# Performance work log

Hardware: AMD Instinct MI355X
Metric: run time of the kernel (lower is better)

## Reference

```python
import jax, jax.numpy as jnp
import numpy as np

LN_EPS = 1e-5

def _ln(x, g, b):
    mu = x.mean(-1, keepdims=True)
    var = ((x - mu) ** 2).mean(-1, keepdims=True)
    return (x - mu) * jax.lax.rsqrt(var + LN_EPS) * g + b

def _gru(x, h, wih, whh, bih, bhh):
    # torch GRUCell: gates ordered (r, z, n)
    gi = x @ wih.T + bih
    gh = h @ whh.T + bhh
    ir, iz, inn = jnp.split(gi, 3, axis=-1)
    hr, hz, hn = jnp.split(gh, 3, axis=-1)
    r = jax.nn.sigmoid(ir + hr)
    z = jax.nn.sigmoid(iz + hz)
    n = jnp.tanh(inn + r * hn)
    return (1.0 - z) * n + z * h

def setup_inputs() -> dict:
    key = jax.random.key(0)
    ks = jax.random.split(key, 10)
    B, N, D, S, H = 64, 4096, 128, 8, 256
    w = D ** -0.5  # weight scale to keep activations sane
    return {
        'inputs': jax.random.normal(ks[0], (B, N, D), jnp.float32),
        'slot_noise': jax.random.normal(ks[1], (1, S, D), jnp.float32),
        'slots_mu': jax.random.normal(ks[2], (1, S, D), jnp.float32) * w,
        'slots_log_sigma': jnp.zeros((1, S, D), jnp.float32),
        'wq': jax.random.normal(ks[3], (D, D), jnp.float32) * w,
        'bq': jnp.zeros((D,), jnp.float32),
        'wk': jax.random.normal(ks[4], (D, D), jnp.float32) * w,
        'bk': jnp.zeros((D,), jnp.float32),
        'wv': jax.random.normal(ks[5], (D, D), jnp.float32) * w,
        'bv': jnp.zeros((D,), jnp.float32),
        'gru_wih': jax.random.normal(ks[6], (3 * D, D), jnp.float32) * w,
        'gru_whh': jax.random.normal(ks[7], (3 * D, D), jnp.float32) * w,
        'gru_bih': jnp.zeros((3 * D,), jnp.float32),
        'gru_bhh': jnp.zeros((3 * D,), jnp.float32),
        'ns_g': jnp.ones((D,), jnp.float32),
        'ns_b': jnp.zeros((D,), jnp.float32),
        'ni_g': jnp.ones((D,), jnp.float32),
        'ni_b': jnp.zeros((D,), jnp.float32),
        'mlp_ln_g': jnp.ones((D,), jnp.float32),
        'mlp_ln_b': jnp.zeros((D,), jnp.float32),
        'mlp_w1': jax.random.normal(ks[8], (H, D), jnp.float32) * w,
        'mlp_b1': jnp.zeros((H,), jnp.float32),
        'mlp_w2': jax.random.normal(ks[9], (D, H), jnp.float32) * (H ** -0.5),
        'mlp_b2': jnp.zeros((D,), jnp.float32),
    }

N_ITERS = 3

def reference(inputs, slot_noise, slots_mu, slots_log_sigma, wq, bq, wk, bk, wv, bv,
              gru_wih, gru_whh, gru_bih, gru_bhh, ns_g, ns_b, ni_g, ni_b,
              mlp_ln_g, mlp_ln_b, mlp_w1, mlp_b1, mlp_w2, mlp_b2):
    B, N, D = inputs.shape
    S = slots_mu.shape[1]
    slots = slots_mu + jnp.exp(slots_log_sigma) * slot_noise  # [1,S,D]
    slots = jnp.broadcast_to(slots, (B, S, D))
    x = _ln(inputs, ni_g, ni_b)
    k = x @ wk.T + bk  # [B,N,D]
    v = x @ wv.T + bv
    scale = 1.0 / jnp.sqrt(jnp.float32(D))
    for _ in range(N_ITERS):
        q = _ln(slots, ns_g, ns_b) @ wq.T + bq  # [B,S,D]
        logits = jnp.einsum('bnd,bsd->bns', k, q) * scale
        attn = jax.nn.softmax(logits, axis=-1)  # softmax over slots
        attn_norm = jnp.clip(attn.sum(axis=1, keepdims=True), 1e-8, None)
        slot_attn = attn / attn_norm
        updates = jnp.einsum('bns,bnd->bsd', slot_attn, v)
        slots = _gru(updates, slots, gru_wih, gru_whh, gru_bih, gru_bhh)
        h = jax.nn.gelu(_ln(slots, mlp_ln_g, mlp_ln_b) @ mlp_w1.T + mlp_b1, approximate=False)
        slots = slots + (h @ mlp_w2.T + mlp_b2)
    return slots
```

## Files before the change

### kernel.cpp

```cpp
#include <hip/hip_runtime.h>
#include <hip/hip_bf16.h>
#include <math.h>

#define Bn 64
#define Nn 4096
#define Dn 128
#define Sn 8
#define Hn 256
#define LN_EPS 1e-5f
#define QSCALE 0.08838834764831845f

typedef __bf16 bf16x8 __attribute__((ext_vector_type(8)));
typedef float f32x4 __attribute__((ext_vector_type(4)));
typedef unsigned short ushort_t;

__device__ __forceinline__ float dot4(float4 a, float4 b) {
    return a.x*b.x + a.y*b.y + a.z*b.z + a.w*b.w;
}
__device__ __forceinline__ ushort_t f2bf(float f) {
    __bf16 b = (__bf16)f;
    ushort_t u; __builtin_memcpy(&u, &b, 2); return u;
}
__device__ __forceinline__ float bf2f(ushort_t u) {
    unsigned int x = ((unsigned int)u) << 16; float f; __builtin_memcpy(&f, &x, 4); return f;
}
__device__ __forceinline__ bf16x8 zero8() {
    bf16x8 z;
    #pragma unroll
    for (int i = 0; i < 8; ++i) z[i] = (__bf16)0.0f;
    return z;
}

__global__ void k_slots_init(const float* __restrict__ mu, const float* __restrict__ ls,
                             const float* __restrict__ noise, float* __restrict__ slots) {
    int i = blockIdx.x * blockDim.x + threadIdx.x;
    if (i < Sn * Dn) {
        float v = mu[i] + __expf(ls[i]) * noise[i];
        #pragma unroll 4
        for (int b = 0; b < Bn; ++b) slots[b * Sn * Dn + i] = v;
    }
}

__global__ void k_wprep(const float* __restrict__ wk, const float* __restrict__ wv,
                        ushort_t* __restrict__ wallT) {
    int o = blockIdx.x * blockDim.x + threadIdx.x;
    if (o < 32768) {
        int e = o & 7;
        int l = (o >> 3) & 15;
        int q = (o >> 7) & 3;
        int k = (o >> 9) & 3;
        int G = o >> 11;
        int row = G * 16 + l;
        int col = k * 32 + q * 8 + e;
        float f = (row < 128) ? wk[row * 128 + col] : wv[(row - 128) * 128 + col];
        wallT[o] = f2bf(f);
    }
}

__global__ __launch_bounds__(512) void k_lnkv_mfma(
    const float* __restrict__ inp, const float* __restrict__ ni_g, const float* __restrict__ ni_b,
    const ushort_t* __restrict__ wallT, const float* __restrict__ bk, const float* __restrict__ bv,
    ushort_t* __restrict__ kout, ushort_t* __restrict__ vout)
{
    __shared__ ushort_t wsh[32768];
    const int t = threadIdx.x;
    const int lane = t & 63;
    const int w = t >> 6;
    const int l15 = lane & 15, q = lane >> 4;
    const int rowbase = blockIdx.x * 128;
    const int row = rowbase + w * 16 + l15;
    const int b_idx = rowbase >> 12;

    #pragma unroll
    for (int i = 0; i < 8; ++i) {
        int off = (i * 512 + t) * 8;
        *(bf16x8*)&wsh[off] = *(const bf16x8*)&wallT[off];
    }

    const float* xr = inp + (size_t)row * Dn + q * 8;
    float4 xv[8];
    #pragma unroll
    for (int c = 0; c < 4; ++c) {
        xv[2*c]   = *(const float4*)(xr + c * 32);
        xv[2*c+1] = *(const float4*)(xr + c * 32 + 4);
    }
    float s = 0.f, sq = 0.f;
    #pragma unroll
    for (int i = 0; i < 8; ++i) {
        float4 x4 = xv[i];
        s  += x4.x + x4.y + x4.z + x4.w;
        sq += x4.x*x4.x + x4.y*x4.y + x4.z*x4.z + x4.w*x4.w;
    }
    s  += __shfl_xor(s, 16);  s  += __shfl_xor(s, 32);
    sq += __shfl_xor(sq, 16); sq += __shfl_xor(sq, 32);
    float mu = s * (1.0f / 128.0f);
    float rs = rsqrtf(sq * (1.0f / 128.0f) - mu * mu + LN_EPS);

    bf16x8 xf[4];
    #pragma unroll
    for (int c = 0; c < 4; ++c) {
        const float* gp = ni_g + c * 32 + q * 8;
        const float* bp = ni_b + c * 32 + q * 8;
        float4 g0 = *(const float4*)gp, g1 = *(const float4*)(gp + 4);
        float4 b0 = *(const float4*)bp, b1 = *(const float4*)(bp + 4);
        bf16x8 f;
        f[0] = (__bf16)((xv[2*c].x   - mu) * rs * g0.x + b0.x);
        f[1] = (__bf16)((xv[2*c].y   - mu) * rs * g0.y + b0.y);
        f[2] = (__bf16)((xv[2*c].z   - mu) * rs * g0.z + b0.z);
        f[3] = (__bf16)((xv[2*c].w   - mu) * rs * g0.w + b0.w);
        f[4] = (__bf16)((xv[2*c+1].x - mu) * rs * g1.x + b1.x);
        f[5] = (__bf16)((xv[2*c+1].y - mu) * rs * g1.y + b1.y);
        f[6] = (__bf16)((xv[2*c+1].z - mu) * rs * g1.z + b1.z);
        f[7] = (__bf16)((xv[2*c+1].w - mu) * rs * g1.w + b1.w);
        xf[c] = f;
    }

    __syncthreads();

    const int nloc0 = (rowbase & 4095) + w * 16 + q * 4;
    #pragma unroll
    for (int ct = 0; ct < 16; ++ct) {
        bf16x8 af[4];
        #pragma unroll
        for (int k4 = 0; k4 < 4; ++k4)
            af[k4] = *(const bf16x8*)&wsh[((ct * 4 + k4) * 64 + lane) * 8];
        f32x4 acc = {0.f, 0.f, 0.f, 0.f};
        if (ct < 8) {
            #pragma unroll
            for (int k4 = 0; k4 < 4; ++k4)
                acc = __builtin_amdgcn_mfma_f32_16x16x32_bf16(af[k4], xf[k4], acc, 0, 0, 0);
            int d0 = ct * 16 + q * 4;
            float4 bia = *(const float4*)&bk[d0];
            ushort4 o = { f2bf(acc[0] + bia.x), f2bf(acc[1] + bia.y),
                          f2bf(acc[2] + bia.z), f2bf(acc[3] + bia.w) };
            size_t off = ((size_t)(((rowbase >> 4) + w) * 4 + (d0 >> 5)) * 64
                          + ((d0 >> 3) & 3) * 16 + l15) * 8 + (d0 & 7);
            *(ushort4*)&kout[off] = o;
        } else {
            #pragma unroll
            for (int k4 = 0; k4 < 4; ++k4)
                acc = __builtin_amdgcn_mfma_f32_16x16x32_bf16(xf[k4], af[k4], acc, 0, 0, 0);
            int dgrp = ct - 8;
            float bb = bv[dgrp * 16 + l15];
            ushort4 o = { f2bf(acc[0] + bb), f2bf(acc[1] + bb),
                          f2bf(acc[2] + bb), f2bf(acc[3] + bb) };
            size_t off = (((size_t)(b_idx * 8 + dgrp) * 128 + (nloc0 >> 5)) * 64
                          + ((nloc0 >> 3) & 3) * 16 + l15) * 8 + (nloc0 & 7);
            *(ushort4*)&vout[off] = o;
        }
    }
}

__global__ __launch_bounds__(256) void k_qproj2(
    const float* __restrict__ slots, const float* __restrict__ ns_g, const float* __restrict__ ns_b,
    const float* __restrict__ wq, const float* __restrict__ bq,
    ushort_t* __restrict__ qb)
{
    __shared__ float lnq[8][128];
    const int t = threadIdx.x;
    const int bs0 = blockIdx.x * 8;
    {
        int r = t >> 5, c = (t & 31) * 4;
        float4 x4 = *(const float4*)&slots[(size_t)(bs0 + r) * Dn + c];
        float s  = x4.x + x4.y + x4.z + x4.w;
        float sq = x4.x*x4.x + x4.y*x4.y + x4.z*x4.z + x4.w*x4.w;
        #pragma unroll
        for (int m = 1; m <= 16; m <<= 1) { s += __shfl_xor(s, m); sq += __shfl_xor(sq, m); }
        float mu = s * (1.0f / 128.0f);
        float rs = rsqrtf(sq * (1.0f / 128.0f) - mu * mu + LN_EPS);
        lnq[r][c+0] = (x4.x - mu) * rs * ns_g[c+0] + ns_b[c+0];
        lnq[r][c+1] = (x4.y - mu) * rs * ns_g[c+1] + ns_b[c+1];
        lnq[r][c+2] = (x4.z - mu) * rs * ns_g[c+2] + ns_b[c+2];
        lnq[r][c+3] = (x4.w - mu) * rs * ns_g[c+3] + ns_b[c+3];
    }
    __syncthreads();
    {
        int c = t & 127, rb = (t >> 7) * 4;
        const float* W = wq + (size_t)c * Dn;
        float acc[4] = {0.f, 0.f, 0.f, 0.f};
        for (int d = 0; d < 128; d += 4) {
            float4 w4 = *(const float4*)(W + d);
            #pragma unroll
            for (int rr = 0; rr < 4; ++rr) acc[rr] += dot4(w4, *(const float4*)&lnq[rb + rr][d]);
        }
        float bb = bq[c];
        #pragma unroll
        for (int rr = 0; rr < 4; ++rr)
            qb[(size_t)(bs0 + rb + rr) * Dn + c] = f2bf((acc[rr] + bb) * QSCALE);
    }
}

__global__ __launch_bounds__(512) void k_attn_mfma(
    const ushort_t* __restrict__ kbuf, const ushort_t* __restrict__ vtbuf,
    const ushort_t* __restrict__ qb,
    float* __restrict__ upart, float* __restrict__ npart)
{
    __shared__ float ush[8][8][128];
    __shared__ float nsh[8][8];
    const int t = threadIdx.x;
    const int b = blockIdx.y;
    const int chunk = blockIdx.x;
    const int lane = t & 63;
    const int w = t >> 6;
    const int l15 = lane & 15, q = lane >> 4;
    const int srcA = ((lane & 16) << 1) | l15;
    const bool hi = lane >= 32;

    bf16x8 aq[4];
    #pragma unroll
    for (int c = 0; c < 4; ++c) {
        bf16x8 z = zero8();
        if (l15 < 8)
            z = *(const bf16x8*)&qb[((size_t)b * Sn + l15) * Dn + c * 32 + q * 8];
        aq[c] = z;
    }

    f32x4 acc[8];
    #pragma unroll
    for (int dg = 0; dg < 8; ++dg) acc[dg] = (f32x4){0.f, 0.f, 0.f, 0.f};
    float nacc = 0.f;

    #pragma unroll
    for (int u = 0; u < 2; ++u) {
        const int n32 = chunk * 512 + w * 64 + u * 32;
        const int ng = n32 >> 4;
        const int nc = n32 >> 5;

        f32x4 lg2[2];
        #pragma unroll
        for (int T = 0; T < 2; ++T) {
            f32x4 lg = {0.f, 0.f, 0.f, 0.f};
            #pragma unroll
            for (int c = 0; c < 4; ++c) {
                bf16x8 kf = *(const bf16x8*)&kbuf[(((size_t)b * 256 + ng + T) * 4 + c) * 512 + lane * 8];
                lg = __builtin_amdgcn_mfma_f32_16x16x32_bf16(kf, aq[c], lg, 0, 0, 0);
            }
            lg2[T] = lg;
        }

        bf16x8 bvf[8];
        #pragma unroll
        for (int dg = 0; dg < 8; ++dg)
            bvf[dg] = *(const bf16x8*)&vtbuf[(((size_t)b * 8 + dg) * 128 + nc) * 512 + lane * 8];

        float p0[4], p1[4];
        #pragma unroll
        for (int T = 0; T < 2; ++T) {
            float* pp = T ? p1 : p0;
            #pragma unroll
            for (int r = 0; r < 4; ++r) {
                float m = lg2[T][r];
                m = fmaxf(m, __shfl_xor(m, 1));
                m = fmaxf(m, __shfl_xor(m, 2));
                m = fmaxf(m, __shfl_xor(m, 4));
                float p = __expf(lg2[T][r] - m);
                float ss = p;
                ss += __shfl_xor(ss, 1); ss += __shfl_xor(ss, 2); ss += __shfl_xor(ss, 4);
                pp[r] = p * (1.0f / ss);
            }
        }
        float paf[8];
        #pragma unroll
        for (int r = 0; r < 4; ++r) {
            float a0 = __shfl(p0[r], srcA);
            float a1 = __shfl(p1[r], srcA);
            float c0 = __shfl(p0[r], srcA + 16);
            float c1 = __shfl(p1[r], srcA + 16);
            paf[r]     = hi ? a1 : a0;
            paf[r + 4] = hi ? c1 : c0;
        }
        bf16x8 pa;
        #pragma unroll
        for (int e = 0; e < 8; ++e) {
            __bf16 bb = (__bf16)paf[e];
            pa[e] = bb;
            nacc += (float)bb;
        }
        #pragma unroll
        for (int dg = 0; dg < 8; ++dg)
            acc[dg] = __builtin_amdgcn_mfma_f32_16x16x32_bf16(pa, bvf[dg], acc[dg], 0, 0, 0);
    }

    nacc += __shfl_xor(nacc, 16);
    nacc += __shfl_xor(nacc, 32);
    if (lane < 8) nsh[w][lane] = nacc;
    if (q < 2) {
        #pragma unroll
        for (int dg = 0; dg < 8; ++dg)
            #pragma unroll
            for (int r = 0; r < 4; ++r)
                ush[w][q * 4 + r][dg * 16 + l15] = acc[dg][r];
    }
    __syncthreads();
    if (t < 256) {
        int s = t >> 5, d0 = (t & 31) * 4;
        float4 sum = {0.f, 0.f, 0.f, 0.f};
        #pragma unroll
        for (int w8 = 0; w8 < 8; ++w8) {
            float4 vv = *(const float4*)&ush[w8][s][d0];
            sum.x += vv.x; sum.y += vv.y; sum.z += vv.z; sum.w += vv.w;
        }
        *(float4*)&upart[((size_t)chunk * 512 + b * 8 + s) * 128 + d0] = sum;
    }
    if (t < 8) {
        float sn = 0.f;
        #pragma unroll
        for (int w8 = 0; w8 < 8; ++w8) sn += nsh[w8][t];
        npart[chunk * 512 + b * 8 + t] = sn;
    }
}

__global__ __launch_bounds__(256) void k_update3(
    const float* __restrict__ slots,
    const float* __restrict__ upart, const float* __restrict__ npart,
    const float* __restrict__ wih, const float* __restrict__ whh,
    const float* __restrict__ bih, const float* __restrict__ bhh,
    const float* __restrict__ mlg, const float* __restrict__ mlb,
    const float* __restrict__ w1, const float* __restrict__ b1,
    const float* __restrict__ w2, const float* __restrict__ b2,
    const float* __restrict__ ns_g, const float* __restrict__ ns_b,
    const float* __restrict__ wq, const float* __restrict__ bq,
    float* __restrict__ outp, ushort_t* __restrict__ qb, int do_q)
{
    __shared__ float us[128];
    __shared__ float hs[128];
    __shared__ float gs[768];
    __shared__ float hnw[128];
    __shared__ float lns[128];
    __shared__ float h1s[256];
    const int t = threadIdx.x;
    const int bs = blockIdx.x;

    if (t < 128) {
        float u = 0.f;
        #pragma unroll
        for (int c = 0; c < 8; ++c) u += upart[((size_t)(c * 512 + bs)) * 128 + t];
        float nsum = 0.f;
        #pragma unroll
        for (int c = 0; c < 8; ++c) nsum += npart[c * 512 + bs];
        us[t] = u / fmaxf(nsum, 1e-8f);
        hs[t] = slots[(size_t)bs * Dn + t];
    }
    __syncthreads();

    #pragma unroll
    for (int jj = 0; jj < 3; ++jj) {
        int j = t + jj * 256;
        const float* W = (j < 384) ? (wih + (size_t)j * Dn) : (whh + (size_t)(j - 384) * Dn);
        const float* X = (j < 384) ? us : hs;
        float a = 0.f;
        #pragma unroll 8
        for (int d = 0; d < 128; d += 4)
            a += dot4(*(const float4*)(W + d), *(const float4*)(X + d));
        gs[j] = a;
    }
    __syncthreads();

    if (t < 64) {
        float hnew[2];
        #pragma unroll
        for (int e = 0; e < 2; ++e) {
            int i = t + e * 64;
            float ir = gs[i]       + bih[i],       hr = gs[384 + i] + bhh[i];
            float iz = gs[128 + i] + bih[128 + i], hz = gs[512 + i] + bhh[128 + i];
            float in_= gs[256 + i] + bih[256 + i], hn = gs[640 + i] + bhh[256 + i];
            float r = 1.0f / (1.0f + __expf(-(ir + hr)));
            float z = 1.0f / (1.0f + __expf(-(iz + hz)));
            float n = tanhf(in_ + r * hn);
            hnew[e] = (1.0f - z) * n + z * hs[i];
        }
        float s  = hnew[0] + hnew[1];
        float sq = hnew[0]*hnew[0] + hnew[1]*hnew[1];
        #pragma unroll
        for (int m = 1; m <= 32; m <<= 1) { s += __shfl_xor(s, m); sq += __shfl_xor(sq, m); }
        float mu = s * (1.0f / 128.0f);
        float rs = rsqrtf(sq * (1.0f / 128.0f) - mu * mu + LN_EPS);
        #pragma unroll
        for (int e = 0; e < 2; ++e) {
            int i = t + e * 64;
            hnw[i] = hnew[e];
            lns[i] = (hnew[e] - mu) * rs * mlg[i] + mlb[i];
        }
    }
    __syncthreads();

    {
        const float* W = w1 + (size_t)t * Dn;
        float a = 0.f;
        #pragma unroll 8
        for (int d = 0; d < 128; d += 4)
            a += dot4(*(const float4*)(W + d), *(const float4*)&lns[d]);
        float x = a + b1[t];
        h1s[t] = 0.5f * x * (1.0f + erff(x * 0.70710678118654752f));
    }
    __syncthreads();

    if (t < 128) {
        const float* W = w2 + (size_t)t * Hn;
        float a = 0.f;
        #pragma unroll 8
        for (int d = 0; d < 256; d += 4)
            a += dot4(*(const float4*)(W + d), *(const float4*)&h1s[d]);
        float o = hnw[t] + a + b2[t];
        outp[(size_t)bs * Dn + t] = o;
        us[t] = o;
    }
    if (do_q) {
        __syncthreads();
        if (t < 64) {
            float v0 = us[t], v1 = us[t + 64];
            float s  = v0 + v1;
            float sq = v0*v0 + v1*v1;
            #pragma unroll
            for (int m = 1; m <= 32; m <<= 1) { s += __shfl_xor(s, m); sq += __shfl_xor(sq, m); }
            float mu = s * (1.0f / 128.0f);
            float rs = rsqrtf(sq * (1.0f / 128.0f) - mu * mu + LN_EPS);
            lns[t]      = (v0 - mu) * rs * ns_g[t]      + ns_b[t];
            lns[t + 64] = (v1 - mu) * rs * ns_g[t + 64] + ns_b[t + 64];
        }
        __syncthreads();
        if (t < 128) {
            const float* W = wq + (size_t)t * Dn;
            float a = 0.f;
            #pragma unroll 8
            for (int d = 0; d < 128; d += 4)
                a += dot4(*(const float4*)(W + d), *(const float4*)&lns[d]);
            qb[(size_t)bs * Dn + t] = f2bf((a + bq[t]) * QSCALE);
        }
    }
}

extern "C" void kernel_launch(void* const* d_in, const int* in_sizes, int n_in,
                              void* d_out, int out_size, void* d_ws, size_t ws_size,
                              hipStream_t stream) {
    (void)in_sizes; (void)n_in; (void)out_size; (void)ws_size;
    const float* inputs   = (const float*)d_in[0];
    const float* noise    = (const float*)d_in[1];
    const float* slots_mu = (const float*)d_in[2];
    const float* slots_ls = (const float*)d_in[3];
    const float* wq  = (const float*)d_in[4];
    const float* bq  = (const float*)d_in[5];
    const float* wk  = (const float*)d_in[6];
    const float* bk  = (const float*)d_in[7];
    const float* wv  = (const float*)d_in[8];
    const float* bv  = (const float*)d_in[9];
    const float* gwih = (const float*)d_in[10];
    const float* gwhh = (const float*)d_in[11];
    const float* gbih = (const float*)d_in[12];
    const float* gbhh = (const float*)d_in[13];
    const float* ns_g = (const float*)d_in[14];
    const float* ns_b = (const float*)d_in[15];
    const float* ni_g = (const float*)d_in[16];
    const float* ni_b = (const float*)d_in[17];
    const float* mlg  = (const float*)d_in[18];
    const float* mlb  = (const float*)d_in[19];
    const float* mw1  = (const float*)d_in[20];
    const float* mb1  = (const float*)d_in[21];
    const float* mw2  = (const float*)d_in[22];
    const float* mb2  = (const float*)d_in[23];

    float* ws      = (float*)d_ws;
    float* slots   = ws;
    float* upart   = ws + 65536;
    float* npart   = ws + 589824;
    ushort_t* qb    = (ushort_t*)(ws + 593920);
    ushort_t* wallT = (ushort_t*)(ws + 626688);
    ushort_t* kbuf  = (ushort_t*)(ws + 643072);
    ushort_t* vtbuf = kbuf + 33554432;

    k_slots_init<<<4, 256, 0, stream>>>(slots_mu, slots_ls, noise, slots);
    k_wprep<<<128, 256, 0, stream>>>(wk, wv, wallT);
    k_lnkv_mfma<<<2048, 512, 0, stream>>>(inputs, ni_g, ni_b, wallT, bk, bv, kbuf, vtbuf);
    k_qproj2<<<64, 256, 0, stream>>>(slots, ns_g, ns_b, wq, bq, qb);
    for (int iter = 0; iter < 3; ++iter) {
        k_attn_mfma<<<dim3(8, 64), 512, 0, stream>>>(kbuf, vtbuf, qb, upart, npart);
        float* outp = (iter == 2) ? (float*)d_out : slots;
        k_update3<<<512, 256, 0, stream>>>(slots, upart, npart, gwih, gwhh, gbih, gbhh,
                                           mlg, mlb, mw1, mb1, mw2, mb2, ns_g, ns_b, wq, bq,
                                           outp, qb, (iter == 2) ? 0 : 1);
    }
}
```

Before: 454.9 us.

## Persist LN+KV projection blocks over four row tiles with input prefetch

The LN+K/V projection kernel now launches 512 blocks, each processing four consecutive 128-row tiles. The 64KB bf16 weight copy into shared memory is done once per four tiles instead of once per tile. The next tile's inputs are prefetched into registers while the current tile is computed. The slot-init and weight-prep kernels are merged into one launch, and launch bounds now request 4 waves per SIMD. This trades fewer blocks and more register pressure for lower LDS-fill cost and load latency hiding.

```diff
diff --git a/kernel.cpp b/kernel.cpp
--- a/kernel.cpp
+++ b/kernel.cpp
@@ -31,20 +31,12 @@
     return z;
 }
 
-__global__ void k_slots_init(const float* __restrict__ mu, const float* __restrict__ ls,
-                             const float* __restrict__ noise, float* __restrict__ slots) {
-    int i = blockIdx.x * blockDim.x + threadIdx.x;
-    if (i < Sn * Dn) {
-        float v = mu[i] + __expf(ls[i]) * noise[i];
-        #pragma unroll 4
-        for (int b = 0; b < Bn; ++b) slots[b * Sn * Dn + i] = v;
-    }
-}
-
-__global__ void k_wprep(const float* __restrict__ wk, const float* __restrict__ wv,
-                        ushort_t* __restrict__ wallT) {
-    int o = blockIdx.x * blockDim.x + threadIdx.x;
-    if (o < 32768) {
+__global__ void k_prep(const float* __restrict__ wk, const float* __restrict__ wv,
+                       ushort_t* __restrict__ wallT,
+                       const float* __restrict__ mu, const float* __restrict__ ls,
+                       const float* __restrict__ noise, float* __restrict__ slots) {
+    if (blockIdx.x < 128) {
+        int o = blockIdx.x * 256 + threadIdx.x;
         int e = o & 7;
         int l = (o >> 3) & 15;
         int q = (o >> 7) & 3;
@@ -54,10 +46,17 @@
         int col = k * 32 + q * 8 + e;
         float f = (row < 128) ? wk[row * 128 + col] : wv[(row - 128) * 128 + col];
         wallT[o] = f2bf(f);
-    }
-}
-
-__global__ __launch_bounds__(512) void k_lnkv_mfma(
+    } else {
+        int i = (blockIdx.x - 128) * 256 + threadIdx.x;
+        if (i < Sn * Dn) {
+            float v = mu[i] + __expf(ls[i]) * noise[i];
+            #pragma unroll 4
+            for (int b = 0; b < Bn; ++b) slots[b * Sn * Dn + i] = v;
+        }
+    }
+}
+
+__global__ __launch_bounds__(512, 4) void k_lnkv_mfma(
     const float* __restrict__ inp, const float* __restrict__ ni_g, const float* __restrict__ ni_b,
     const ushort_t* __restrict__ wallT, const float* __restrict__ bk, const float* __restrict__ bv,
     ushort_t* __restrict__ kout, ushort_t* __restrict__ vout)
@@ -67,87 +66,106 @@
     const int lane = t & 63;
     const int w = t >> 6;
     const int l15 = lane & 15, q = lane >> 4;
-    const int rowbase = blockIdx.x * 128;
-    const int row = rowbase + w * 16 + l15;
-    const int b_idx = rowbase >> 12;
-
+    const int g0 = blockIdx.x * 4;
+    const int rowoff = w * 16 + l15;
+
+    float4 xv[8];
+    {
+        const float* xr = inp + (size_t)(g0 * 128 + rowoff) * Dn + q * 8;
+        #pragma unroll
+        for (int c = 0; c < 4; ++c) {
+            xv[2*c]   = *(const float4*)(xr + c * 32);
+            xv[2*c+1] = *(const float4*)(xr + c * 32 + 4);
+        }
+    }
     #pragma unroll
     for (int i = 0; i < 8; ++i) {
         int off = (i * 512 + t) * 8;
         *(bf16x8*)&wsh[off] = *(const bf16x8*)&wallT[off];
     }
-
-    const float* xr = inp + (size_t)row * Dn + q * 8;
-    float4 xv[8];
-    #pragma unroll
-    for (int c = 0; c < 4; ++c) {
-        xv[2*c]   = *(const float4*)(xr + c * 32);
-        xv[2*c+1] = *(const float4*)(xr + c * 32 + 4);
-    }
-    float s = 0.f, sq = 0.f;
-    #pragma unroll
-    for (int i = 0; i < 8; ++i) {
-        float4 x4 = xv[i];
-        s  += x4.x + x4.y + x4.z + x4.w;
-        sq += x4.x*x4.x + x4.y*x4.y + x4.z*x4.z + x4.w*x4.w;
-    }
-    s  += __shfl_xor(s, 16);  s  += __shfl_xor(s, 32);
-    sq += __shfl_xor(sq, 16); sq += __shfl_xor(sq, 32);
-    float mu = s * (1.0f / 128.0f);
-    float rs = rsqrtf(sq * (1.0f / 128.0f) - mu * mu + LN_EPS);
-
-    bf16x8 xf[4];
-    #pragma unroll
-    for (int c = 0; c < 4; ++c) {
-        const float* gp = ni_g + c * 32 + q * 8;
-        const float* bp = ni_b + c * 32 + q * 8;
-        float4 g0 = *(const float4*)gp, g1 = *(const float4*)(gp + 4);
-        float4 b0 = *(const float4*)bp, b1 = *(const float4*)(bp + 4);
-        bf16x8 f;
-        f[0] = (__bf16)((xv[2*c].x   - mu) * rs * g0.x + b0.x);
-        f[1] = (__bf16)((xv[2*c].y   - mu) * rs * g0.y + b0.y);
-        f[2] = (__bf16)((xv[2*c].z   - mu) * rs * g0.z + b0.z);
-        f[3] = (__bf16)((xv[2*c].w   - mu) * rs * g0.w + b0.w);
-        f[4] = (__bf16)((xv[2*c+1].x - mu) * rs * g1.x + b1.x);
-        f[5] = (__bf16)((xv[2*c+1].y - mu) * rs * g1.y + b1.y);
-        f[6] = (__bf16)((xv[2*c+1].z - mu) * rs * g1.z + b1.z);
-        f[7] = (__bf16)((xv[2*c+1].w - mu) * rs * g1.w + b1.w);
-        xf[c] = f;
-    }
-
-    __syncthreads();
-
-    const int nloc0 = (rowbase & 4095) + w * 16 + q * 4;
-    #pragma unroll
-    for (int ct = 0; ct < 16; ++ct) {
-        bf16x8 af[4];
-        #pragma unroll
-        for (int k4 = 0; k4 < 4; ++k4)
-            af[k4] = *(const bf16x8*)&wsh[((ct * 4 + k4) * 64 + lane) * 8];
-        f32x4 acc = {0.f, 0.f, 0.f, 0.f};
-        if (ct < 8) {
+    __syncthreads();
+
+    #pragma unroll
+    for (int g = 0; g < 4; ++g) {
+        const int rowbase = (g0 + g) * 128;
+        const int b_idx = rowbase >> 12;
+
+        float4 xvn[8];
+        if (g < 3) {
+            const float* xr = inp + (size_t)(rowbase + 128 + rowoff) * Dn + q * 8;
+            #pragma unroll
+            for (int c = 0; c < 4; ++c) {
+                xvn[2*c]   = *(const float4*)(xr + c * 32);
+                xvn[2*c+1] = *(const float4*)(xr + c * 32 + 4);
+            }
+        }
+
+        float s = 0.f, sq = 0.f;
+        #pragma unroll
+        for (int i = 0; i < 8; ++i) {
+            float4 x4 = xv[i];
+            s  += x4.x + x4.y + x4.z + x4.w;
+            sq += x4.x*x4.x + x4.y*x4.y + x4.z*x4.z + x4.w*x4.w;
+        }
+        s  += __shfl_xor(s, 16);  s  += __shfl_xor(s, 32);
+        sq += __shfl_xor(sq, 16); sq += __shfl_xor(sq, 32);
+        float mu = s * (1.0f / 128.0f);
+        float rs = rsqrtf(sq * (1.0f / 128.0f) - mu * mu + LN_EPS);
+
+        bf16x8 xf[4];
+        #pragma unroll
+        for (int c = 0; c < 4; ++c) {
+            const float* gp = ni_g + c * 32 + q * 8;
+            const float* bp = ni_b + c * 32 + q * 8;
+            float4 g0v = *(const float4*)gp, g1 = *(const float4*)(gp + 4);
+            float4 b0 = *(const float4*)bp, b1 = *(const float4*)(bp + 4);
+            bf16x8 f;
+            f[0] = (__bf16)((xv[2*c].x   - mu) * rs * g0v.x + b0.x);
+            f[1] = (__bf16)((xv[2*c].y   - mu) * rs * g0v.y + b0.y);
+            f[2] = (__bf16)((xv[2*c].z   - mu) * rs * g0v.z + b0.z);
+            f[3] = (__bf16)((xv[2*c].w   - mu) * rs * g0v.w + b0.w);
+            f[4] = (__bf16)((xv[2*c+1].x - mu) * rs * g1.x + b1.x);
+            f[5] = (__bf16)((xv[2*c+1].y - mu) * rs * g1.y + b1.y);
+            f[6] = (__bf16)((xv[2*c+1].z - mu) * rs * g1.z + b1.z);
+            f[7] = (__bf16)((xv[2*c+1].w - mu) * rs * g1.w + b1.w);
+            xf[c] = f;
+        }
+
+        const int nloc0 = (rowbase & 4095) + w * 16 + q * 4;
+        #pragma unroll
+        for (int ct = 0; ct < 16; ++ct) {
+            bf16x8 af[4];
             #pragma unroll
             for (int k4 = 0; k4 < 4; ++k4)
-                acc = __builtin_amdgcn_mfma_f32_16x16x32_bf16(af[k4], xf[k4], acc, 0, 0, 0);
-            int d0 = ct * 16 + q * 4;
-            float4 bia = *(const float4*)&bk[d0];
-            ushort4 o = { f2bf(acc[0] + bia.x), f2bf(acc[1] + bia.y),
-                          f2bf(acc[2] + bia.z), f2bf(acc[3] + bia.w) };
-            size_t off = ((size_t)(((rowbase >> 4) + w) * 4 + (d0 >> 5)) * 64
-                          + ((d0 >> 3) & 3) * 16 + l15) * 8 + (d0 & 7);
-            *(ushort4*)&kout[off] = o;
-        } else {
-            #pragma unroll
-            for (int k4 = 0; k4 < 4; ++k4)
-                acc = __builtin_amdgcn_mfma_f32_16x16x32_bf16(xf[k4], af[k4], acc, 0, 0, 0);
-            int dgrp = ct - 8;
-            float bb = bv[dgrp * 16 + l15];
-            ushort4 o = { f2bf(acc[0] + bb), f2bf(acc[1] + bb),
-                          f2bf(acc[2] + bb), f2bf(acc[3] + bb) };
-            size_t off = (((size_t)(b_idx * 8 + dgrp) * 128 + (nloc0 >> 5)) * 64
-                          + ((nloc0 >> 3) & 3) * 16 + l15) * 8 + (nloc0 & 7);
-            *(ushort4*)&vout[off] = o;
-        }
+                af[k4] = *(const bf16x8*)&wsh[((ct * 4 + k4) * 64 + lane) * 8];
+            f32x4 acc = {0.f, 0.f, 0.f, 0.f};
+            if (ct < 8) {
+                #pragma unroll
+                for (int k4 = 0; k4 < 4; ++k4)
+                    acc = __builtin_amdgcn_mfma_f32_16x16x32_bf16(af[k4], xf[k4], acc, 0, 0, 0);
+                int d0 = ct * 16 + q * 4;
+                float4 bia = *(const float4*)&bk[d0];
+                ushort4 o = { f2bf(acc[0] + bia.x), f2bf(acc[1] + bia.y),
+                              f2bf(acc[2] + bia.z), f2bf(acc[3] + bia.w) };
+                size_t off = ((size_t)(((rowbase >> 4) + w) * 4 + (d0 >> 5)) * 64
+                              + ((d0 >> 3) & 3) * 16 + l15) * 8 + (d0 & 7);
+                *(ushort4*)&kout[off] = o;
+            } else {
+                #pragma unroll
+                for (int k4 = 0; k4 < 4; ++k4)
+                    acc = __builtin_amdgcn_mfma_f32_16x16x32_bf16(xf[k4], af[k4], acc, 0, 0, 0);
+                int dgrp = ct - 8;
+                float bb = bv[dgrp * 16 + l15];
+                ushort4 o = { f2bf(acc[0] + bb), f2bf(acc[1] + bb),
+                              f2bf(acc[2] + bb), f2bf(acc[3] + bb) };
+                size_t off = (((size_t)(b_idx * 8 + dgrp) * 128 + (nloc0 >> 5)) * 64
+                              + ((nloc0 >> 3) & 3) * 16 + l15) * 8 + (nloc0 & 7);
+                *(ushort4*)&vout[off] = o;
+            }
+        }
+
+        #pragma unroll
+        for (int i = 0; i < 8; ++i) xv[i] = xvn[i];
     }
 }
 
@@ -468,9 +486,8 @@
     ushort_t* kbuf  = (ushort_t*)(ws + 643072);
     ushort_t* vtbuf = kbuf + 33554432;
 
-    k_slots_init<<<4, 256, 0, stream>>>(slots_mu, slots_ls, noise, slots);
-    k_wprep<<<128, 256, 0, stream>>>(wk, wv, wallT);
-    k_lnkv_mfma<<<2048, 512, 0, stream>>>(inputs, ni_g, ni_b, wallT, bk, bv, kbuf, vtbuf);
+    k_prep<<<132, 256, 0, stream>>>(wk, wv, wallT, slots_mu, slots_ls, noise, slots);
+    k_lnkv_mfma<<<512, 512, 0, stream>>>(inputs, ni_g, ni_b, wallT, bk, bv, kbuf, vtbuf);
     k_qproj2<<<64, 256, 0, stream>>>(slots, ns_g, ns_b, wq, bq, qb);
     for (int iter = 0; iter < 3; ++iter) {
         k_attn_mfma<<<dim3(8, 64), 512, 0, stream>>>(kbuf, vtbuf, qb, upart, npart);
```

After: 578.4 us. 1.27x slower.

## Split attention into more chunks, enlarge LN+KV blocks, merge prep kernels

Applied to the files above, without the earlier changes.

The attention kernel now processes 256 tokens per block with one 32-token tile per wave instead of two, and the grid doubles to 16 chunks per batch. This raises parallelism at the cost of more partial sums for the update kernel to reduce. The LN+KV projection kernel now uses 1024-thread blocks covering 256 rows, which halves the number of times the shared bf16 weight tile is loaded. It also issues the input loads before the weight copy to overlap them. The slot-init and weight-prep kernels are merged into one launch.

```diff
diff --git a/kernel.cpp b/kernel.cpp
--- a/kernel.cpp
+++ b/kernel.cpp
@@ -9,6 +9,7 @@
 #define Hn 256
 #define LN_EPS 1e-5f
 #define QSCALE 0.08838834764831845f
+#define NCHUNK 16
 
 typedef __bf16 bf16x8 __attribute__((ext_vector_type(8)));
 typedef float f32x4 __attribute__((ext_vector_type(4)));
@@ -21,9 +22,6 @@
     __bf16 b = (__bf16)f;
     ushort_t u; __builtin_memcpy(&u, &b, 2); return u;
 }
-__device__ __forceinline__ float bf2f(ushort_t u) {
-    unsigned int x = ((unsigned int)u) << 16; float f; __builtin_memcpy(&f, &x, 4); return f;
-}
 __device__ __forceinline__ bf16x8 zero8() {
     bf16x8 z;
     #pragma unroll
@@ -31,20 +29,12 @@
     return z;
 }
 
-__global__ void k_slots_init(const float* __restrict__ mu, const float* __restrict__ ls,
-                             const float* __restrict__ noise, float* __restrict__ slots) {
-    int i = blockIdx.x * blockDim.x + threadIdx.x;
-    if (i < Sn * Dn) {
-        float v = mu[i] + __expf(ls[i]) * noise[i];
-        #pragma unroll 4
-        for (int b = 0; b < Bn; ++b) slots[b * Sn * Dn + i] = v;
-    }
-}
-
-__global__ void k_wprep(const float* __restrict__ wk, const float* __restrict__ wv,
-                        ushort_t* __restrict__ wallT) {
-    int o = blockIdx.x * blockDim.x + threadIdx.x;
-    if (o < 32768) {
+__global__ void k_prep(const float* __restrict__ wk, const float* __restrict__ wv,
+                       ushort_t* __restrict__ wallT,
+                       const float* __restrict__ mu, const float* __restrict__ ls,
+                       const float* __restrict__ noise, float* __restrict__ slots) {
+    if (blockIdx.x < 128) {
+        int o = blockIdx.x * 256 + threadIdx.x;
         int e = o & 7;
         int l = (o >> 3) & 15;
         int q = (o >> 7) & 3;
@@ -54,10 +44,17 @@
         int col = k * 32 + q * 8 + e;
         float f = (row < 128) ? wk[row * 128 + col] : wv[(row - 128) * 128 + col];
         wallT[o] = f2bf(f);
-    }
-}
-
-__global__ __launch_bounds__(512) void k_lnkv_mfma(
+    } else {
+        int i = (blockIdx.x - 128) * 256 + threadIdx.x;
+        if (i < Sn * Dn) {
+            float v = mu[i] + __expf(ls[i]) * noise[i];
+            #pragma unroll 4
+            for (int b = 0; b < Bn; ++b) slots[b * Sn * Dn + i] = v;
+        }
+    }
+}
+
+__global__ __launch_bounds__(1024) void k_lnkv_mfma(
     const float* __restrict__ inp, const float* __restrict__ ni_g, const float* __restrict__ ni_b,
     const ushort_t* __restrict__ wallT, const float* __restrict__ bk, const float* __restrict__ bv,
     ushort_t* __restrict__ kout, ushort_t* __restrict__ vout)
@@ -67,15 +64,9 @@
     const int lane = t & 63;
     const int w = t >> 6;
     const int l15 = lane & 15, q = lane >> 4;
-    const int rowbase = blockIdx.x * 128;
+    const int rowbase = blockIdx.x * 256;
     const int row = rowbase + w * 16 + l15;
     const int b_idx = rowbase >> 12;
-
-    #pragma unroll
-    for (int i = 0; i < 8; ++i) {
-        int off = (i * 512 + t) * 8;
-        *(bf16x8*)&wsh[off] = *(const bf16x8*)&wallT[off];
-    }
 
     const float* xr = inp + (size_t)row * Dn + q * 8;
     float4 xv[8];
@@ -84,6 +75,12 @@
         xv[2*c]   = *(const float4*)(xr + c * 32);
         xv[2*c+1] = *(const float4*)(xr + c * 32 + 4);
     }
+    #pragma unroll
+    for (int i = 0; i < 4; ++i) {
+        int off = (i * 1024 + t) * 8;
+        *(bf16x8*)&wsh[off] = *(const bf16x8*)&wallT[off];
+    }
+
     float s = 0.f, sq = 0.f;
     #pragma unroll
     for (int i = 0; i < 8; ++i) {
@@ -215,70 +212,66 @@
         aq[c] = z;
     }
 
+    const int n32 = chunk * 256 + w * 32;
+    const int ng = n32 >> 4;
+    const int nc = n32 >> 5;
+
+    f32x4 lg2[2];
+    #pragma unroll
+    for (int T = 0; T < 2; ++T) {
+        f32x4 lg = {0.f, 0.f, 0.f, 0.f};
+        #pragma unroll
+        for (int c = 0; c < 4; ++c) {
+            bf16x8 kf = *(const bf16x8*)&kbuf[(((size_t)b * 256 + ng + T) * 4 + c) * 512 + lane * 8];
+            lg = __builtin_amdgcn_mfma_f32_16x16x32_bf16(kf, aq[c], lg, 0, 0, 0);
+        }
+        lg2[T] = lg;
+    }
+
+    bf16x8 bvf[8];
+    #pragma unroll
+    for (int dg = 0; dg < 8; ++dg)
+        bvf[dg] = *(const bf16x8*)&vtbuf[(((size_t)b * 8 + dg) * 128 + nc) * 512 + lane * 8];
+
+    float p0[4], p1[4];
+    #pragma unroll
+    for (int T = 0; T < 2; ++T) {
+        float* pp = T ? p1 : p0;
+        #pragma unroll
+        for (int r = 0; r < 4; ++r) {
+            float m = lg2[T][r];
+            m = fmaxf(m, __shfl_xor(m, 1));
+            m = fmaxf(m, __shfl_xor(m, 2));
+            m = fmaxf(m, __shfl_xor(m, 4));
+            float p = __expf(lg2[T][r] - m);
+            float ss = p;
+            ss += __shfl_xor(ss, 1); ss += __shfl_xor(ss, 2); ss += __shfl_xor(ss, 4);
+            pp[r] = p * (1.0f / ss);
+        }
+    }
+    float paf[8];
+    float nacc = 0.f;
+    #pragma unroll
+    for (int r = 0; r < 4; ++r) {
+        float a0 = __shfl(p0[r], srcA);
+        float a1 = __shfl(p1[r], srcA);
+        float c0 = __shfl(p0[r], srcA + 16);
+        float c1 = __shfl(p1[r], srcA + 16);
+        paf[r]     = hi ? a1 : a0;
+        paf[r + 4] = hi ? c1 : c0;
+    }
+    bf16x8 pa;
+    #pragma unroll
+    for (int e = 0; e < 8; ++e) {
+        __bf16 bb = (__bf16)paf[e];
+        pa[e] = bb;
+        nacc += (float)bb;
+    }
     f32x4 acc[8];
     #pragma unroll
-    for (int dg = 0; dg < 8; ++dg) acc[dg] = (f32x4){0.f, 0.f, 0.f, 0.f};
-    float nacc = 0.f;
-
-    #pragma unroll
-    for (int u = 0; u < 2; ++u) {
-        const int n32 = chunk * 512 + w * 64 + u * 32;
-        const int ng = n32 >> 4;
-        const int nc = n32 >> 5;
-
-        f32x4 lg2[2];
-        #pragma unroll
-        for (int T = 0; T < 2; ++T) {
-            f32x4 lg = {0.f, 0.f, 0.f, 0.f};
-            #pragma unroll
-            for (int c = 0; c < 4; ++c) {
-                bf16x8 kf = *(const bf16x8*)&kbuf[(((size_t)b * 256 + ng + T) * 4 + c) * 512 + lane * 8];
-                lg = __builtin_amdgcn_mfma_f32_16x16x32_bf16(kf, aq[c], lg, 0, 0, 0);
-            }
-            lg2[T] = lg;
-        }
-
-        bf16x8 bvf[8];
-        #pragma unroll
-        for (int dg = 0; dg < 8; ++dg)
-            bvf[dg] = *(const bf16x8*)&vtbuf[(((size_t)b * 8 + dg) * 128 + nc) * 512 + lane * 8];
-
-        float p0[4], p1[4];
-        #pragma unroll
-        for (int T = 0; T < 2; ++T) {
-            float* pp = T ? p1 : p0;
-            #pragma unroll
-            for (int r = 0; r < 4; ++r) {
-                float m = lg2[T][r];
-                m = fmaxf(m, __shfl_xor(m, 1));
-                m = fmaxf(m, __shfl_xor(m, 2));
-                m = fmaxf(m, __shfl_xor(m, 4));
-                float p = __expf(lg2[T][r] - m);
-                float ss = p;
-                ss += __shfl_xor(ss, 1); ss += __shfl_xor(ss, 2); ss += __shfl_xor(ss, 4);
-                pp[r] = p * (1.0f / ss);
-            }
-        }
-        float paf[8];
-        #pragma unroll
-        for (int r = 0; r < 4; ++r) {
-            float a0 = __shfl(p0[r], srcA);
-            float a1 = __shfl(p1[r], srcA);
-            float c0 = __shfl(p0[r], srcA + 16);
-            float c1 = __shfl(p1[r], srcA + 16);
-            paf[r]     = hi ? a1 : a0;
-            paf[r + 4] = hi ? c1 : c0;
-        }
-        bf16x8 pa;
-        #pragma unroll
-        for (int e = 0; e < 8; ++e) {
-            __bf16 bb = (__bf16)paf[e];
-            pa[e] = bb;
-            nacc += (float)bb;
-        }
-        #pragma unroll
-        for (int dg = 0; dg < 8; ++dg)
-            acc[dg] = __builtin_amdgcn_mfma_f32_16x16x32_bf16(pa, bvf[dg], acc[dg], 0, 0, 0);
+    for (int dg = 0; dg < 8; ++dg) {
+        acc[dg] = (f32x4){0.f, 0.f, 0.f, 0.f};
+        acc[dg] = __builtin_amdgcn_mfma_f32_16x16x32_bf16(pa, bvf[dg], acc[dg], 0, 0, 0);
     }
 
     nacc += __shfl_xor(nacc, 16);
@@ -334,10 +327,10 @@
     if (t < 128) {
         float u = 0.f;
         #pragma unroll
-        for (int c = 0; c < 8; ++c) u += upart[((size_t)(c * 512 + bs)) * 128 + t];
+        for (int c = 0; c < NCHUNK; ++c) u += upart[((size_t)(c * 512 + bs)) * 128 + t];
         float nsum = 0.f;
         #pragma unroll
-        for (int c = 0; c < 8; ++c) nsum += npart[c * 512 + bs];
+        for (int c = 0; c < NCHUNK; ++c) nsum += npart[c * 512 + bs];
         us[t] = u / fmaxf(nsum, 1e-8f);
         hs[t] = slots[(size_t)bs * Dn + t];
     }
@@ -462,18 +455,17 @@
     float* ws      = (float*)d_ws;
     float* slots   = ws;
     float* upart   = ws + 65536;
-    float* npart   = ws + 589824;
-    ushort_t* qb    = (ushort_t*)(ws + 593920);
-    ushort_t* wallT = (ushort_t*)(ws + 626688);
-    ushort_t* kbuf  = (ushort_t*)(ws + 643072);
+    float* npart   = ws + 1114112;
+    ushort_t* qb    = (ushort_t*)(ws + 1122304);
+    ushort_t* wallT = (ushort_t*)(ws + 1155072);
+    ushort_t* kbuf  = (ushort_t*)(ws + 1171456);
     ushort_t* vtbuf = kbuf + 33554432;
 
-    k_slots_init<<<4, 256, 0, stream>>>(slots_mu, slots_ls, noise, slots);
-    k_wprep<<<128, 256, 0, stream>>>(wk, wv, wallT);
-    k_lnkv_mfma<<<2048, 512, 0, stream>>>(inputs, ni_g, ni_b, wallT, bk, bv, kbuf, vtbuf);
+    k_prep<<<132, 256, 0, stream>>>(wk, wv, wallT, slots_mu, slots_ls, noise, slots);
+    k_lnkv_mfma<<<1024, 1024, 0, stream>>>(inputs, ni_g, ni_b, wallT, bk, bv, kbuf, vtbuf);
     k_qproj2<<<64, 256, 0, stream>>>(slots, ns_g, ns_b, wq, bq, qb);
     for (int iter = 0; iter < 3; ++iter) {
-        k_attn_mfma<<<dim3(8, 64), 512, 0, stream>>>(kbuf, vtbuf, qb, upart, npart);
+        k_attn_mfma<<<dim3(NCHUNK, 64), 512, 0, stream>>>(kbuf, vtbuf, qb, upart, npart);
         float* outp = (iter == 2) ? (float*)d_out : slots;
         k_update3<<<512, 256, 0, stream>>>(slots, upart, npart, gwih, gwhh, gbih, gbhh,
                                            mlg, mlb, mw1, mb1, mw2, mb2, ns_g, ns_b, wq, bq,
```

Result: no change. 462.4 us (+1.7%).
